# Performance work log

Measured on AMD Instinct MI355X. Metric: run time of the kernel, lower is better.

Reference implementation:

```python
import jax, jax.numpy as jnp
import numpy as np

H = 16          # ATTENTION_HEAD
E = 300         # EXPANSION_LENGTH
D = 768         # TEXT_EMBEDDING_DIM
HD = D // H     # 48


def setup_inputs() -> dict:
    key = jax.random.key(0)
    ks = jax.random.split(key, 10)
    b, n, ql, kl = 1, 4, 64, 64
    q = jax.random.normal(ks[0], (b, n, ql, D), dtype=jnp.float32)
    k = jax.random.normal(ks[1], (b, 1, kl, D), dtype=jnp.float32)
    v = jax.random.normal(ks[2], (b, 1, kl, D), dtype=jnp.float32)
    s = 1.0 / np.sqrt(D)
    Wq = jax.random.normal(ks[3], (D, D), dtype=jnp.float32) * s
    bq = jnp.zeros((D,), dtype=jnp.float32)
    Wk = jax.random.normal(ks[4], (D, D), dtype=jnp.float32) * s
    bk = jnp.zeros((D,), dtype=jnp.float32)
    Wv = jax.random.normal(ks[5], (D, D), dtype=jnp.float32) * s
    bv = jnp.zeros((D,), dtype=jnp.float32)
    memory = jax.random.normal(ks[6], (1, E, H, HD), dtype=jnp.float32) * 0.05
    return {"q": q, "k": k, "v": v, "Wq": Wq, "bq": bq, "Wk": Wk,
            "bk": bk, "Wv": Wv, "bv": bv, "memory": memory}


def reference(q, k, v, Wq, bq, Wk, bk, Wv, bv, memory):
    b, n, ql, _ = q.shape
    kl = k.shape[2]
    # Dense projections
    Q = (q @ Wq + bq).reshape(b, n, ql, H, HD)          # bnqhd
    K = (k @ Wk + bk).reshape(b, kl, H, HD)             # bkhd
    V = (v @ Wv + bv).reshape(b, kl, H, HD)             # bkhd
    # memory (1,E,H,HD) -> (1,E,1,H,HD); K -> (b,1,kl,H,HD); broadcast sum
    broad_sum = memory[:, :, None, :, :] + K[:, None, :, :, :]   # bekhd
    M = jax.nn.relu(jnp.einsum('bekhd,bnqhd->bnekqh', broad_sum, Q))
    E_seq = jnp.einsum('bnekqh,bkhd->bnekhd', M, V)
    out = jnp.einsum('bnekhd,bnekqh->bnqhd', E_seq, M)
    return out.reshape(q.shape)
```

## Files before the change

### kernel.cpp

```cpp
#include <hip/hip_runtime.h>

#define H   16
#define E   300
#define D   768
#define HD  48
#define QL  64
#define KL  64
#define NH  64
#define ROWS 384
#define SPLITK 12
#define NCH 16

#define OFF_PP 0
#define OFF_PF (SPLITK*ROWS*D)
#define OFF_A  (OFF_PF + ROWS*D)
#define OFF_B  (OFF_A + NH*E*QL)
#define OFF_SP (OFF_B + NH*KL*QL)

__global__ __launch_bounds__(256, 1) void proj_kernel(
    const float* __restrict__ qin, const float* __restrict__ kin, const float* __restrict__ vin,
    const float* __restrict__ Wq, const float* __restrict__ Wk, const float* __restrict__ Wv,
    float* __restrict__ ws)
{
    const int rowblk = blockIdx.x;
    const int col0   = blockIdx.y * 128;
    const int ks     = blockIdx.z;
    const int kbase  = ks * 64;

    const int g0 = rowblk * 128;
    const float* Wlo = (g0      < 256) ? Wq : (g0      < 320) ? Wk : Wv;
    const float* Whi = (g0 + 64 < 256) ? Wq : (g0 + 64 < 320) ? Wk : Wv;

    __shared__ float XsT[32][132];
    __shared__ float Ws2[2][32][128];

    const int tid = threadIdx.x;
    const int r0  = (tid >> 4) * 8;
    const int c0  = (tid & 15) * 8;
    const int hw  = r0 >> 6;

    float acc[8][8];
    #pragma unroll
    for (int i = 0; i < 8; i++)
        #pragma unroll
        for (int j = 0; j < 8; j++) acc[i][j] = 0.f;

    for (int kk2 = 0; kk2 < 64; kk2 += 32) {
        #pragma unroll
        for (int it = 0; it < 4; it++) {
            const int idx = it * 256 + tid;
            const int row = idx >> 3;
            const int d4  = (idx & 7) * 4;
            const int grow = rowblk * 128 + row;
            const float* src = (grow < 256) ? (qin + grow * D)
                             : (grow < 320) ? (kin + (grow - 256) * D)
                                            : (vin + (grow - 320) * D);
            const float4 xv = *(const float4*)(src + kbase + kk2 + d4);
            XsT[d4 + 0][row] = xv.x; XsT[d4 + 1][row] = xv.y;
            XsT[d4 + 2][row] = xv.z; XsT[d4 + 3][row] = xv.w;
        }
        #pragma unroll
        for (int it = 0; it < 8; it++) {
            const int idx  = it * 256 + tid;
            const int half = idx >> 10;
            const int rem  = idx & 1023;
            const int dk   = rem >> 5;
            const int c4   = (rem & 31) * 4;
            const float* Wsel = half ? Whi : Wlo;
            *(float4*)&Ws2[half][dk][c4] =
                *(const float4*)(Wsel + (kbase + kk2 + dk) * D + col0 + c4);
        }
        __syncthreads();
        #pragma unroll
        for (int dk = 0; dk < 32; dk++) {
            const float4 x0 = *(const float4*)&XsT[dk][r0];
            const float4 x1 = *(const float4*)&XsT[dk][r0 + 4];
            const float4 w0 = *(const float4*)&Ws2[hw][dk][c0];
            const float4 w1 = *(const float4*)&Ws2[hw][dk][c0 + 4];
            const float xr[8] = {x0.x, x0.y, x0.z, x0.w, x1.x, x1.y, x1.z, x1.w};
            const float wc[8] = {w0.x, w0.y, w0.z, w0.w, w1.x, w1.y, w1.z, w1.w};
            #pragma unroll
            for (int i = 0; i < 8; i++)
                #pragma unroll
                for (int j = 0; j < 8; j++)
                    acc[i][j] = fmaf(xr[i], wc[j], acc[i][j]);
        }
        __syncthreads();
    }
    float* P = ws + OFF_PP + ks * (ROWS * D);
    #pragma unroll
    for (int i = 0; i < 8; i++) {
        float* base = P + (rowblk * 128 + r0 + i) * D + col0 + c0;
        *(float4*)(base)     = make_float4(acc[i][0], acc[i][1], acc[i][2], acc[i][3]);
        *(float4*)(base + 4) = make_float4(acc[i][4], acc[i][5], acc[i][6], acc[i][7]);
    }
}

__global__ __launch_bounds__(256) void reduce_kernel(
    const float* __restrict__ bq, const float* __restrict__ bk, const float* __restrict__ bv,
    float* __restrict__ ws)
{
    const int idx = (blockIdx.x * 256 + threadIdx.x) * 4;
    const float* PP = ws + OFF_PP;
    float4 v = *(const float4*)(PP + idx);
    #pragma unroll
    for (int c = 1; c < SPLITK; c++) {
        const float4 p = *(const float4*)(PP + c * (ROWS * D) + idx);
        v.x += p.x; v.y += p.y; v.z += p.z; v.w += p.w;
    }
    const int row = idx / D, col = idx % D;
    const float* bias = (row < 256) ? bq : (row < 320) ? bk : bv;
    const float4 b = *(const float4*)(bias + col);
    v.x += b.x; v.y += b.y; v.z += b.z; v.w += b.w;
    *(float4*)(ws + OFF_PF + idx) = v;
}

__global__ __launch_bounds__(256) void ab_kernel(
    const float* __restrict__ memo, float* __restrict__ ws)
{
    const int nh = blockIdx.x;
    const int rg = blockIdx.y;
    const int n = nh >> 4, h = nh & 15;
    const float* Pf = ws + OFF_PF;
    float* A = ws + OFF_A;
    float* B = ws + OFF_B;

    __shared__ float RsT[48][132];
    __shared__ float QsT[48][68];

    const int tid = threadIdx.x;
    #pragma unroll
    for (int it = 0; it < 6; it++) {
        const int idx = it * 256 + tid;
        const int row = idx / 12;
        const int d4  = (idx % 12) * 4;
        const int rr = rg * 128 + row;
        float4 rv = make_float4(0.f, 0.f, 0.f, 0.f);
        if (rr < E)            rv = *(const float4*)(memo + rr * D + h * HD + d4);
        else if (rr < E + KL)  rv = *(const float4*)(Pf + (256 + rr - E) * D + h * HD + d4);
        RsT[d4 + 0][row] = rv.x; RsT[d4 + 1][row] = rv.y;
        RsT[d4 + 2][row] = rv.z; RsT[d4 + 3][row] = rv.w;
    }
    #pragma unroll
    for (int it = 0; it < 3; it++) {
        const int idx = it * 256 + tid;
        const int q  = idx / 12;
        const int d4 = (idx % 12) * 4;
        const float4 qv = *(const float4*)(Pf + (n * QL + q) * D + h * HD + d4);
        QsT[d4 + 0][q] = qv.x; QsT[d4 + 1][q] = qv.y;
        QsT[d4 + 2][q] = qv.z; QsT[d4 + 3][q] = qv.w;
    }
    __syncthreads();

    const int r0 = (tid >> 4) * 8;
    const int q0 = (tid & 15) * 4;
    float acc[8][4];
    #pragma unroll
    for (int i = 0; i < 8; i++)
        #pragma unroll
        for (int j = 0; j < 4; j++) acc[i][j] = 0.f;

    #pragma unroll 4
    for (int d = 0; d < HD; d++) {
        const float4 rf0 = *(const float4*)&RsT[d][r0];
        const float4 rf1 = *(const float4*)&RsT[d][r0 + 4];
        const float4 qf  = *(const float4*)&QsT[d][q0];
        const float rr8[8] = {rf0.x, rf0.y, rf0.z, rf0.w, rf1.x, rf1.y, rf1.z, rf1.w};
        const float qq4[4] = {qf.x, qf.y, qf.z, qf.w};
        #pragma unroll
        for (int i = 0; i < 8; i++)
            #pragma unroll
            for (int j = 0; j < 4; j++)
                acc[i][j] = fmaf(rr8[i], qq4[j], acc[i][j]);
    }
    #pragma unroll
    for (int i = 0; i < 8; i++) {
        const int rr = rg * 128 + r0 + i;
        const float4 av = make_float4(acc[i][0], acc[i][1], acc[i][2], acc[i][3]);
        if (rr < E)            *(float4*)(A + (nh * E + rr) * QL + q0) = av;
        else if (rr < E + KL)  *(float4*)(B + (nh * KL + (rr - E)) * QL + q0) = av;
    }
}

__global__ __launch_bounds__(256, 1) void main_kernel(float* __restrict__ ws)
{
    const int nh = blockIdx.x;
    const int cg = blockIdx.y;
    const int tid = threadIdx.x;
    const int lane = tid & 63;
    const int w = tid >> 6;

    __shared__ float As[75 * 64];
    __shared__ float Bs[64][68];

    const float* Ag = ws + OFF_A + (nh * E + cg * 75) * QL;
    for (int idx = tid; idx < 1200; idx += 256)
        *(float4*)&As[idx * 4] = *(const float4*)(Ag + idx * 4);
    const float* Bg = ws + OFF_B + nh * (KL * QL);
    #pragma unroll
    for (int it = 0; it < 4; it++) {
        const int idx = it * 256 + tid;
        const int k  = idx >> 4;
        const int q4 = (idx & 15) * 4;
        *(float4*)&Bs[k][q4] = *(const float4*)(Bg + idx * 4);
    }
    __syncthreads();

    float b[64];
    #pragma unroll
    for (int j = 0; j < 16; j++)
        *(float4*)&b[j * 4] = *(const float4*)&Bs[lane][j * 4];

    float s[64];
    #pragma unroll
    for (int j = 0; j < 64; j++) s[j] = 0.f;

    const int eBeg = w * 19;
    const int eEnd = (eBeg + 19 < 75) ? eBeg + 19 : 75;
    for (int e = eBeg; e < eEnd; e++) {
        float m[64];
        #pragma unroll
        for (int j4 = 0; j4 < 16; j4++) {
            const float4 a = *(const float4*)&As[e * 64 + j4 * 4];
            m[j4 * 4 + 0] = fmaxf(a.x + b[j4 * 4 + 0], 0.f);
            m[j4 * 4 + 1] = fmaxf(a.y + b[j4 * 4 + 1], 0.f);
            m[j4 * 4 + 2] = fmaxf(a.z + b[j4 * 4 + 2], 0.f);
            m[j4 * 4 + 3] = fmaxf(a.w + b[j4 * 4 + 3], 0.f);
        }
        float p0 = 0.f, p1 = 0.f, p2 = 0.f, p3 = 0.f;
        #pragma unroll
        for (int j4 = 0; j4 < 16; j4++) {
            p0 += m[j4 * 4 + 0]; p1 += m[j4 * 4 + 1];
            p2 += m[j4 * 4 + 2]; p3 += m[j4 * 4 + 3];
        }
        const float p = (p0 + p1) + (p2 + p3);
        #pragma unroll
        for (int j = 0; j < 64; j++)
            s[j] = fmaf(m[j], p, s[j]);
    }

    float* Sp = ws + OFF_SP + (((cg * 4 + w) * NH + nh) * QL) * KL;
    #pragma unroll
    for (int q = 0; q < 64; q++)
        Sp[q * KL + lane] = s[q];
}

__global__ __launch_bounds__(256) void out_kernel(
    const float* __restrict__ ws_c, float* __restrict__ outp)
{
    const int nh = blockIdx.x;
    const int qq = blockIdx.y;
    const int n = nh >> 4, h = nh & 15;
    const int q0 = qq * 16;
    const float* Sp = ws_c + OFF_SP;
    const float* Pf = ws_c + OFF_PF;

    __shared__ float S_l[16][64];
    __shared__ float V_l[64][52];

    const int tid = threadIdx.x;
    #pragma unroll
    for (int it = 0; it < 4; it++) {
        const int idx = it * 256 + tid;
        const int qi = idx >> 6, k = idx & 63;
        float sum = 0.f;
        #pragma unroll
        for (int c = 0; c < NCH; c++)
            sum += Sp[((c * NH + nh) * QL + q0 + qi) * KL + k];
        S_l[qi][k] = sum;
    }
    #pragma unroll
    for (int it = 0; it < 3; it++) {
        const int idx = it * 256 + tid;
        const int k  = idx / 12;
        const int d4 = (idx % 12) * 4;
        *(float4*)&V_l[k][d4] = *(const float4*)(Pf + (320 + k) * D + h * HD + d4);
    }
    __syncthreads();

    const int qi = tid >> 4;
    const int dg = tid & 15;
    if (dg < 12) {
        float a0 = 0.f, a1 = 0.f, a2 = 0.f, a3 = 0.f;
        #pragma unroll 8
        for (int k = 0; k < KL; k++) {
            const float sv = S_l[qi][k];
            const float4 vf = *(const float4*)&V_l[k][dg * 4];
            a0 = fmaf(sv, vf.x, a0); a1 = fmaf(sv, vf.y, a1);
            a2 = fmaf(sv, vf.z, a2); a3 = fmaf(sv, vf.w, a3);
        }
        *(float4*)(outp + (n * QL + q0 + qi) * D + h * HD + dg * 4) =
            make_float4(a0, a1, a2, a3);
    }
}

extern "C" void kernel_launch(void* const* d_in, const int* in_sizes, int n_in,
                              void* d_out, int out_size, void* d_ws, size_t ws_size,
                              hipStream_t stream)
{
    const float* q    = (const float*)d_in[0];
    const float* k    = (const float*)d_in[1];
    const float* v    = (const float*)d_in[2];
    const float* Wq   = (const float*)d_in[3];
    const float* bq   = (const float*)d_in[4];
    const float* Wk   = (const float*)d_in[5];
    const float* bk   = (const float*)d_in[6];
    const float* Wv   = (const float*)d_in[7];
    const float* bv   = (const float*)d_in[8];
    const float* memo = (const float*)d_in[9];
    float* ws   = (float*)d_ws;
    float* outp = (float*)d_out;

    hipLaunchKernelGGL(proj_kernel, dim3(3, 6, 12), dim3(256), 0, stream,
                       q, k, v, Wq, Wk, Wv, ws);
    hipLaunchKernelGGL(reduce_kernel, dim3(288), dim3(256), 0, stream, bq, bk, bv, ws);
    hipLaunchKernelGGL(ab_kernel, dim3(64, 3), dim3(256), 0, stream, memo, ws);
    hipLaunchKernelGGL(main_kernel, dim3(64, 4), dim3(256), 0, stream, ws);
    hipLaunchKernelGGL(out_kernel, dim3(64, 4), dim3(256), 0, stream, ws, outp);
}
```

Measured before the change: 124.5 us.

## Fuse split-K reduction into consumers and stream operands from global memory

Drops the separate reduce kernel. The split-K partial sums plus bias are now summed directly where Q, K and V are consumed, in the ab and out kernels. The projection kernel reads X rows directly from global memory instead of transposing them into shared memory. The ab kernel streams memory rows from global memory, and main_kernel reads A rows from global memory with double-buffered registers instead of staging them in shared memory. This removes one launch and a full write/read of the reduced projections, at the cost of redundant 12-way partial reads repeated across blocks and higher register pressure.

```diff
diff --git a/kernel.cpp b/kernel.cpp
--- a/kernel.cpp
+++ b/kernel.cpp
@@ -9,11 +9,10 @@
 #define NH  64
 #define ROWS 384
 #define SPLITK 12
-#define NCH 16
+#define NCHUNK 16
 
 #define OFF_PP 0
-#define OFF_PF (SPLITK*ROWS*D)
-#define OFF_A  (OFF_PF + ROWS*D)
+#define OFF_A  (SPLITK*ROWS*D)
 #define OFF_B  (OFF_A + NH*E*QL)
 #define OFF_SP (OFF_B + NH*KL*QL)
 
@@ -26,18 +25,27 @@
     const int col0   = blockIdx.y * 128;
     const int ks     = blockIdx.z;
     const int kbase  = ks * 64;
-
-    const int g0 = rowblk * 128;
-    const float* Wlo = (g0      < 256) ? Wq : (g0      < 320) ? Wk : Wv;
-    const float* Whi = (g0 + 64 < 256) ? Wq : (g0 + 64 < 320) ? Wk : Wv;
-
-    __shared__ float XsT[32][132];
+    const int g0     = rowblk * 128;
+
+    const float* Wlo = (g0      < 256) ? Wq : Wk;
+    const float* Whi = (g0 + 64 < 256) ? Wq : Wv;
+
     __shared__ float Ws2[2][32][128];
 
-    const int tid = threadIdx.x;
-    const int r0  = (tid >> 4) * 8;
-    const int c0  = (tid & 15) * 8;
-    const int hw  = r0 >> 6;
+    const int tid  = threadIdx.x;
+    const int half = tid >> 7;
+    const int loc  = tid & 127;
+    const int r0a  = (loc >> 4) * 4;
+    const int c0a  = (loc & 15) * 4;
+
+    const float* xp[8];
+    #pragma unroll
+    for (int i = 0; i < 8; i++) {
+        const int r = g0 + half * 64 + r0a + (i < 4 ? i : 28 + i);
+        xp[i] = ((r < 256) ? (qin + r * D)
+               : (r < 320) ? (kin + (r - 256) * D)
+                           : (vin + (r - 320) * D)) + kbase;
+    }
 
     float acc[8][8];
     #pragma unroll
@@ -47,140 +55,187 @@
 
     for (int kk2 = 0; kk2 < 64; kk2 += 32) {
         #pragma unroll
-        for (int it = 0; it < 4; it++) {
+        for (int it = 0; it < 8; it++) {
             const int idx = it * 256 + tid;
-            const int row = idx >> 3;
-            const int d4  = (idx & 7) * 4;
-            const int grow = rowblk * 128 + row;
-            const float* src = (grow < 256) ? (qin + grow * D)
-                             : (grow < 320) ? (kin + (grow - 256) * D)
-                                            : (vin + (grow - 320) * D);
-            const float4 xv = *(const float4*)(src + kbase + kk2 + d4);
-            XsT[d4 + 0][row] = xv.x; XsT[d4 + 1][row] = xv.y;
-            XsT[d4 + 2][row] = xv.z; XsT[d4 + 3][row] = xv.w;
-        }
-        #pragma unroll
-        for (int it = 0; it < 8; it++) {
-            const int idx  = it * 256 + tid;
-            const int half = idx >> 10;
-            const int rem  = idx & 1023;
-            const int dk   = rem >> 5;
-            const int c4   = (rem & 31) * 4;
-            const float* Wsel = half ? Whi : Wlo;
-            *(float4*)&Ws2[half][dk][c4] =
-                *(const float4*)(Wsel + (kbase + kk2 + dk) * D + col0 + c4);
+            const int s   = idx >> 10;
+            const int rem = idx & 1023;
+            const int dk  = rem >> 5;
+            const int c4  = (rem & 31) * 4;
+            *(float4*)&Ws2[s][dk][c4] =
+                *(const float4*)((s ? Whi : Wlo) + (kbase + kk2 + dk) * D + col0 + c4);
         }
         __syncthreads();
         #pragma unroll
-        for (int dk = 0; dk < 32; dk++) {
-            const float4 x0 = *(const float4*)&XsT[dk][r0];
-            const float4 x1 = *(const float4*)&XsT[dk][r0 + 4];
-            const float4 w0 = *(const float4*)&Ws2[hw][dk][c0];
-            const float4 w1 = *(const float4*)&Ws2[hw][dk][c0 + 4];
-            const float xr[8] = {x0.x, x0.y, x0.z, x0.w, x1.x, x1.y, x1.z, x1.w};
-            const float wc[8] = {w0.x, w0.y, w0.z, w0.w, w1.x, w1.y, w1.z, w1.w};
+        for (int dk4 = 0; dk4 < 8; dk4++) {
+            float4 xv[8];
             #pragma unroll
             for (int i = 0; i < 8; i++)
+                xv[i] = *(const float4*)(xp[i] + kk2 + dk4 * 4);
+            #pragma unroll
+            for (int t = 0; t < 4; t++) {
+                const float4 wa = *(const float4*)&Ws2[half][dk4 * 4 + t][c0a];
+                const float4 wb = *(const float4*)&Ws2[half][dk4 * 4 + t][c0a + 64];
+                const float wc[8] = {wa.x, wa.y, wa.z, wa.w, wb.x, wb.y, wb.z, wb.w};
                 #pragma unroll
-                for (int j = 0; j < 8; j++)
-                    acc[i][j] = fmaf(xr[i], wc[j], acc[i][j]);
+                for (int i = 0; i < 8; i++) {
+                    const float xs = ((const float*)&xv[i])[t];
+                    #pragma unroll
+                    for (int j = 0; j < 8; j++)
+                        acc[i][j] = fmaf(xs, wc[j], acc[i][j]);
+                }
+            }
         }
         __syncthreads();
     }
     float* P = ws + OFF_PP + ks * (ROWS * D);
     #pragma unroll
     for (int i = 0; i < 8; i++) {
-        float* base = P + (rowblk * 128 + r0 + i) * D + col0 + c0;
-        *(float4*)(base)     = make_float4(acc[i][0], acc[i][1], acc[i][2], acc[i][3]);
-        *(float4*)(base + 4) = make_float4(acc[i][4], acc[i][5], acc[i][6], acc[i][7]);
-    }
-}
-
-__global__ __launch_bounds__(256) void reduce_kernel(
-    const float* __restrict__ bq, const float* __restrict__ bk, const float* __restrict__ bv,
+        const int row = g0 + half * 64 + r0a + (i < 4 ? i : 28 + i);
+        *(float4*)(P + row * D + col0 + c0a) =
+            make_float4(acc[i][0], acc[i][1], acc[i][2], acc[i][3]);
+        *(float4*)(P + row * D + col0 + c0a + 64) =
+            make_float4(acc[i][4], acc[i][5], acc[i][6], acc[i][7]);
+    }
+}
+
+__global__ __launch_bounds__(256, 1) void ab_kernel(
+    const float* __restrict__ memo,
+    const float* __restrict__ bq_, const float* __restrict__ bk_,
     float* __restrict__ ws)
-{
-    const int idx = (blockIdx.x * 256 + threadIdx.x) * 4;
-    const float* PP = ws + OFF_PP;
-    float4 v = *(const float4*)(PP + idx);
-    #pragma unroll
-    for (int c = 1; c < SPLITK; c++) {
-        const float4 p = *(const float4*)(PP + c * (ROWS * D) + idx);
-        v.x += p.x; v.y += p.y; v.z += p.z; v.w += p.w;
-    }
-    const int row = idx / D, col = idx % D;
-    const float* bias = (row < 256) ? bq : (row < 320) ? bk : bv;
-    const float4 b = *(const float4*)(bias + col);
-    v.x += b.x; v.y += b.y; v.z += b.z; v.w += b.w;
-    *(float4*)(ws + OFF_PF + idx) = v;
-}
-
-__global__ __launch_bounds__(256) void ab_kernel(
-    const float* __restrict__ memo, float* __restrict__ ws)
 {
     const int nh = blockIdx.x;
     const int rg = blockIdx.y;
     const int n = nh >> 4, h = nh & 15;
-    const float* Pf = ws + OFF_PF;
+    const float* PP = ws + OFF_PP;
     float* A = ws + OFF_A;
     float* B = ws + OFF_B;
 
+    __shared__ float QsT[48][68];
     __shared__ float RsT[48][132];
-    __shared__ float QsT[48][68];
 
     const int tid = threadIdx.x;
-    #pragma unroll
-    for (int it = 0; it < 6; it++) {
-        const int idx = it * 256 + tid;
-        const int row = idx / 12;
-        const int d4  = (idx % 12) * 4;
-        const int rr = rg * 128 + row;
-        float4 rv = make_float4(0.f, 0.f, 0.f, 0.f);
-        if (rr < E)            rv = *(const float4*)(memo + rr * D + h * HD + d4);
-        else if (rr < E + KL)  rv = *(const float4*)(Pf + (256 + rr - E) * D + h * HD + d4);
-        RsT[d4 + 0][row] = rv.x; RsT[d4 + 1][row] = rv.y;
-        RsT[d4 + 2][row] = rv.z; RsT[d4 + 3][row] = rv.w;
-    }
-    #pragma unroll
-    for (int it = 0; it < 3; it++) {
-        const int idx = it * 256 + tid;
-        const int q  = idx / 12;
-        const int d4 = (idx % 12) * 4;
-        const float4 qv = *(const float4*)(Pf + (n * QL + q) * D + h * HD + d4);
-        QsT[d4 + 0][q] = qv.x; QsT[d4 + 1][q] = qv.y;
-        QsT[d4 + 2][q] = qv.z; QsT[d4 + 3][q] = qv.w;
+    for (int l = tid; l < 64 * 12; l += 256) {
+        const int q  = l / 12;
+        const int d4 = (l % 12) * 4;
+        float4 s = make_float4(0.f, 0.f, 0.f, 0.f);
+        #pragma unroll
+        for (int c = 0; c < SPLITK; c++) {
+            const float4 p = *(const float4*)(PP + c * (ROWS * D) + (n * QL + q) * D + h * HD + d4);
+            s.x += p.x; s.y += p.y; s.z += p.z; s.w += p.w;
+        }
+        const float4 bb = *(const float4*)(bq_ + h * HD + d4);
+        QsT[d4 + 0][q] = s.x + bb.x; QsT[d4 + 1][q] = s.y + bb.y;
+        QsT[d4 + 2][q] = s.z + bb.z; QsT[d4 + 3][q] = s.w + bb.w;
+    }
+    if (rg == 2) {
+        for (int l = tid; l < 128 * 12; l += 256) {
+            const int rr = l / 12;
+            const int d4 = (l % 12) * 4;
+            float4 s = make_float4(0.f, 0.f, 0.f, 0.f);
+            if (rr < 44) {
+                s = *(const float4*)(memo + ((256 + rr) * H + h) * HD + d4);
+            } else if (rr < 108) {
+                #pragma unroll
+                for (int c = 0; c < SPLITK; c++) {
+                    const float4 p = *(const float4*)(PP + c * (ROWS * D) + (256 + rr - 44) * D + h * HD + d4);
+                    s.x += p.x; s.y += p.y; s.z += p.z; s.w += p.w;
+                }
+                const float4 bb = *(const float4*)(bk_ + h * HD + d4);
+                s.x += bb.x; s.y += bb.y; s.z += bb.z; s.w += bb.w;
+            }
+            RsT[d4 + 0][rr] = s.x; RsT[d4 + 1][rr] = s.y;
+            RsT[d4 + 2][rr] = s.z; RsT[d4 + 3][rr] = s.w;
+        }
     }
     __syncthreads();
 
-    const int r0 = (tid >> 4) * 8;
-    const int q0 = (tid & 15) * 4;
+    const int r0a = (tid >> 4) * 4;
+    const int q0  = (tid & 15) * 4;
     float acc[8][4];
     #pragma unroll
     for (int i = 0; i < 8; i++)
         #pragma unroll
         for (int j = 0; j < 4; j++) acc[i][j] = 0.f;
 
-    #pragma unroll 4
-    for (int d = 0; d < HD; d++) {
-        const float4 rf0 = *(const float4*)&RsT[d][r0];
-        const float4 rf1 = *(const float4*)&RsT[d][r0 + 4];
-        const float4 qf  = *(const float4*)&QsT[d][q0];
-        const float rr8[8] = {rf0.x, rf0.y, rf0.z, rf0.w, rf1.x, rf1.y, rf1.z, rf1.w};
-        const float qq4[4] = {qf.x, qf.y, qf.z, qf.w};
-        #pragma unroll
-        for (int i = 0; i < 8; i++)
-            #pragma unroll
-            for (int j = 0; j < 4; j++)
-                acc[i][j] = fmaf(rr8[i], qq4[j], acc[i][j]);
-    }
+    if (rg < 2) {
+        const float* mp[8];
+        #pragma unroll
+        for (int i = 0; i < 8; i++) {
+            const int row = rg * 128 + r0a + (i < 4 ? i : 28 + i);
+            mp[i] = memo + (row * H + h) * HD;
+        }
+        #pragma unroll
+        for (int d4 = 0; d4 < 12; d4++) {
+            float4 xv[8];
+            #pragma unroll
+            for (int i = 0; i < 8; i++) xv[i] = *(const float4*)(mp[i] + d4 * 4);
+            #pragma unroll
+            for (int t = 0; t < 4; t++) {
+                const float4 qv = *(const float4*)&QsT[d4 * 4 + t][q0];
+                #pragma unroll
+                for (int i = 0; i < 8; i++) {
+                    const float xs = ((const float*)&xv[i])[t];
+                    acc[i][0] = fmaf(xs, qv.x, acc[i][0]);
+                    acc[i][1] = fmaf(xs, qv.y, acc[i][1]);
+                    acc[i][2] = fmaf(xs, qv.z, acc[i][2]);
+                    acc[i][3] = fmaf(xs, qv.w, acc[i][3]);
+                }
+            }
+        }
+    } else {
+        #pragma unroll 4
+        for (int d = 0; d < 48; d++) {
+            const float4 r0v = *(const float4*)&RsT[d][r0a];
+            const float4 r1v = *(const float4*)&RsT[d][r0a + 64];
+            const float4 qv  = *(const float4*)&QsT[d][q0];
+            const float rr8[8] = {r0v.x, r0v.y, r0v.z, r0v.w, r1v.x, r1v.y, r1v.z, r1v.w};
+            #pragma unroll
+            for (int i = 0; i < 8; i++) {
+                acc[i][0] = fmaf(rr8[i], qv.x, acc[i][0]);
+                acc[i][1] = fmaf(rr8[i], qv.y, acc[i][1]);
+                acc[i][2] = fmaf(rr8[i], qv.z, acc[i][2]);
+                acc[i][3] = fmaf(rr8[i], qv.w, acc[i][3]);
+            }
+        }
+    }
+
     #pragma unroll
     for (int i = 0; i < 8; i++) {
-        const int rr = rg * 128 + r0 + i;
+        const int rloc = r0a + (i < 4 ? i : 60 + i);
         const float4 av = make_float4(acc[i][0], acc[i][1], acc[i][2], acc[i][3]);
-        if (rr < E)            *(float4*)(A + (nh * E + rr) * QL + q0) = av;
-        else if (rr < E + KL)  *(float4*)(B + (nh * KL + (rr - E)) * QL + q0) = av;
-    }
-}
+        if (rg < 2) {
+            *(float4*)(A + (nh * E + rg * 128 + rloc) * QL + q0) = av;
+        } else {
+            if (rloc < 44)        *(float4*)(A + (nh * E + 256 + rloc) * QL + q0) = av;
+            else if (rloc < 108)  *(float4*)(B + (nh * KL + (rloc - 44)) * QL + q0) = av;
+        }
+    }
+}
+
+__device__ __forceinline__ void loadA16(float4* dst, const float* src) {
+    #pragma unroll
+    for (int j = 0; j < 16; j++) dst[j] = *(const float4*)(src + j * 4);
+}
+
+#define MAIN_STEP(AB) do {                                                  \
+    float m[64];                                                            \
+    _Pragma("unroll")                                                       \
+    for (int j4 = 0; j4 < 16; j4++) {                                       \
+        const float4 a = (AB)[j4];                                          \
+        m[j4*4+0] = fmaxf(a.x + b[j4*4+0], 0.f);                            \
+        m[j4*4+1] = fmaxf(a.y + b[j4*4+1], 0.f);                            \
+        m[j4*4+2] = fmaxf(a.z + b[j4*4+2], 0.f);                            \
+        m[j4*4+3] = fmaxf(a.w + b[j4*4+3], 0.f);                            \
+    }                                                                       \
+    float p0 = 0.f, p1 = 0.f, p2 = 0.f, p3 = 0.f;                           \
+    _Pragma("unroll")                                                       \
+    for (int j4 = 0; j4 < 16; j4++) {                                       \
+        p0 += m[j4*4+0]; p1 += m[j4*4+1]; p2 += m[j4*4+2]; p3 += m[j4*4+3]; \
+    }                                                                       \
+    const float p = (p0 + p1) + (p2 + p3);                                  \
+    _Pragma("unroll")                                                       \
+    for (int j = 0; j < 64; j++) s[j] = fmaf(m[j], p, s[j]);                \
+} while (0)
 
 __global__ __launch_bounds__(256, 1) void main_kernel(float* __restrict__ ws)
 {
@@ -189,92 +244,76 @@
     const int tid = threadIdx.x;
     const int lane = tid & 63;
     const int w = tid >> 6;
-
-    __shared__ float As[75 * 64];
-    __shared__ float Bs[64][68];
-
-    const float* Ag = ws + OFF_A + (nh * E + cg * 75) * QL;
-    for (int idx = tid; idx < 1200; idx += 256)
-        *(float4*)&As[idx * 4] = *(const float4*)(Ag + idx * 4);
-    const float* Bg = ws + OFF_B + nh * (KL * QL);
-    #pragma unroll
-    for (int it = 0; it < 4; it++) {
-        const int idx = it * 256 + tid;
-        const int k  = idx >> 4;
-        const int q4 = (idx & 15) * 4;
-        *(float4*)&Bs[k][q4] = *(const float4*)(Bg + idx * 4);
-    }
-    __syncthreads();
-
+    const int chunk = cg * 4 + w;
+    const int e0 = chunk * 19;
+    const int e1 = (e0 + 19 < E) ? e0 + 19 : E;
+
+    const float* Bg = ws + OFF_B + (nh * KL + lane) * QL;
     float b[64];
     #pragma unroll
     for (int j = 0; j < 16; j++)
-        *(float4*)&b[j * 4] = *(const float4*)&Bs[lane][j * 4];
+        *(float4*)&b[j * 4] = *(const float4*)(Bg + j * 4);
 
     float s[64];
     #pragma unroll
     for (int j = 0; j < 64; j++) s[j] = 0.f;
 
-    const int eBeg = w * 19;
-    const int eEnd = (eBeg + 19 < 75) ? eBeg + 19 : 75;
-    for (int e = eBeg; e < eEnd; e++) {
-        float m[64];
-        #pragma unroll
-        for (int j4 = 0; j4 < 16; j4++) {
-            const float4 a = *(const float4*)&As[e * 64 + j4 * 4];
-            m[j4 * 4 + 0] = fmaxf(a.x + b[j4 * 4 + 0], 0.f);
-            m[j4 * 4 + 1] = fmaxf(a.y + b[j4 * 4 + 1], 0.f);
-            m[j4 * 4 + 2] = fmaxf(a.z + b[j4 * 4 + 2], 0.f);
-            m[j4 * 4 + 3] = fmaxf(a.w + b[j4 * 4 + 3], 0.f);
-        }
-        float p0 = 0.f, p1 = 0.f, p2 = 0.f, p3 = 0.f;
-        #pragma unroll
-        for (int j4 = 0; j4 < 16; j4++) {
-            p0 += m[j4 * 4 + 0]; p1 += m[j4 * 4 + 1];
-            p2 += m[j4 * 4 + 2]; p3 += m[j4 * 4 + 3];
-        }
-        const float p = (p0 + p1) + (p2 + p3);
-        #pragma unroll
-        for (int j = 0; j < 64; j++)
-            s[j] = fmaf(m[j], p, s[j]);
-    }
-
-    float* Sp = ws + OFF_SP + (((cg * 4 + w) * NH + nh) * QL) * KL;
+    const float* Ag = ws + OFF_A + nh * (E * QL);
+    float4 A0[16], A1[16];
+    loadA16(A0, Ag + e0 * QL);
+    int e = e0;
+    while (true) {
+        if (e + 1 < e1) loadA16(A1, Ag + (e + 1) * QL);
+        MAIN_STEP(A0);
+        e++;
+        if (e >= e1) break;
+        if (e + 1 < e1) loadA16(A0, Ag + (e + 1) * QL);
+        MAIN_STEP(A1);
+        e++;
+        if (e >= e1) break;
+    }
+
+    float* Sp = ws + OFF_SP + (chunk * NH + nh) * (QL * KL);
     #pragma unroll
     for (int q = 0; q < 64; q++)
         Sp[q * KL + lane] = s[q];
 }
 
-__global__ __launch_bounds__(256) void out_kernel(
-    const float* __restrict__ ws_c, float* __restrict__ outp)
+__global__ __launch_bounds__(256, 1) void out_kernel(
+    const float* __restrict__ ws_c, const float* __restrict__ bv_, float* __restrict__ outp)
 {
     const int nh = blockIdx.x;
     const int qq = blockIdx.y;
     const int n = nh >> 4, h = nh & 15;
     const int q0 = qq * 16;
     const float* Sp = ws_c + OFF_SP;
-    const float* Pf = ws_c + OFF_PF;
-
-    __shared__ float S_l[16][64];
+    const float* PP = ws_c + OFF_PP;
+
+    __shared__ float S_l[16][65];
     __shared__ float V_l[64][52];
 
     const int tid = threadIdx.x;
+    for (int l = tid; l < 64 * 12; l += 256) {
+        const int k  = l / 12;
+        const int d4 = (l % 12) * 4;
+        float4 s = make_float4(0.f, 0.f, 0.f, 0.f);
+        #pragma unroll
+        for (int c = 0; c < SPLITK; c++) {
+            const float4 p = *(const float4*)(PP + c * (ROWS * D) + (320 + k) * D + h * HD + d4);
+            s.x += p.x; s.y += p.y; s.z += p.z; s.w += p.w;
+        }
+        const float4 bb = *(const float4*)(bv_ + h * HD + d4);
+        *(float4*)&V_l[k][d4] = make_float4(s.x + bb.x, s.y + bb.y, s.z + bb.z, s.w + bb.w);
+    }
     #pragma unroll
     for (int it = 0; it < 4; it++) {
         const int idx = it * 256 + tid;
         const int qi = idx >> 6, k = idx & 63;
         float sum = 0.f;
         #pragma unroll
-        for (int c = 0; c < NCH; c++)
+        for (int c = 0; c < NCHUNK; c++)
             sum += Sp[((c * NH + nh) * QL + q0 + qi) * KL + k];
         S_l[qi][k] = sum;
-    }
-    #pragma unroll
-    for (int it = 0; it < 3; it++) {
-        const int idx = it * 256 + tid;
-        const int k  = idx / 12;
-        const int d4 = (idx % 12) * 4;
-        *(float4*)&V_l[k][d4] = *(const float4*)(Pf + (320 + k) * D + h * HD + d4);
     }
     __syncthreads();
 
@@ -313,8 +352,7 @@
 
     hipLaunchKernelGGL(proj_kernel, dim3(3, 6, 12), dim3(256), 0, stream,
                        q, k, v, Wq, Wk, Wv, ws);
-    hipLaunchKernelGGL(reduce_kernel, dim3(288), dim3(256), 0, stream, bq, bk, bv, ws);
-    hipLaunchKernelGGL(ab_kernel, dim3(64, 3), dim3(256), 0, stream, memo, ws);
+    hipLaunchKernelGGL(ab_kernel, dim3(64, 3), dim3(256), 0, stream, memo, bq, bk, ws);
     hipLaunchKernelGGL(main_kernel, dim3(64, 4), dim3(256), 0, stream, ws);
-    hipLaunchKernelGGL(out_kernel, dim3(64, 4), dim3(256), 0, stream, ws, outp);
-}
+    hipLaunchKernelGGL(out_kernel, dim3(64, 4), dim3(256), 0, stream, ws, bv, outp);
+}
```

After: 157.9 us. +26.8%, slower.

## Fuse all stages into one cooperative persistent kernel with grid syncs

Applied to the files above, without the earlier changes.

Replaces the five back-to-back launches with a single cooperative kernel of 256 blocks that runs projection, split-K reduction, A/B products, the main accumulation and the output stage, separated by grid.sync(). The aim is to remove per-launch overhead and the idle gaps between kernels, using a shared-memory union so each phase reuses the same LDS. The projection thread mapping is also reworked so each half of the block handles one weight half, with strided rows and columns. A fallback path folds the reduction into ab_kernel and out_kernel in case the cooperative launch fails. Grid-wide barriers carry their own cost and force all 256 blocks to be co-resident.

```diff
diff --git a/kernel.cpp b/kernel.cpp
--- a/kernel.cpp
+++ b/kernel.cpp
@@ -1,4 +1,7 @@
 #include <hip/hip_runtime.h>
+#include <hip/hip_cooperative_groups.h>
+
+namespace cg = cooperative_groups;
 
 #define H   16
 #define E   300
@@ -9,13 +12,14 @@
 #define NH  64
 #define ROWS 384
 #define SPLITK 12
-#define NCH 16
+#define NCHUNK 16
 
 #define OFF_PP 0
 #define OFF_PF (SPLITK*ROWS*D)
 #define OFF_A  (OFF_PF + ROWS*D)
 #define OFF_B  (OFF_A + NH*E*QL)
 #define OFF_SP (OFF_B + NH*KL*QL)
+
 
 __global__ __launch_bounds__(256, 1) void proj_kernel(
     const float* __restrict__ qin, const float* __restrict__ kin, const float* __restrict__ vin,
@@ -26,18 +30,19 @@
     const int col0   = blockIdx.y * 128;
     const int ks     = blockIdx.z;
     const int kbase  = ks * 64;
-
-    const int g0 = rowblk * 128;
-    const float* Wlo = (g0      < 256) ? Wq : (g0      < 320) ? Wk : Wv;
-    const float* Whi = (g0 + 64 < 256) ? Wq : (g0 + 64 < 320) ? Wk : Wv;
+    const int g0     = rowblk * 128;
+
+    const float* Wlo = (g0      < 256) ? Wq : Wk;
+    const float* Whi = (g0 + 64 < 256) ? Wq : Wv;
 
     __shared__ float XsT[32][132];
     __shared__ float Ws2[2][32][128];
 
-    const int tid = threadIdx.x;
-    const int r0  = (tid >> 4) * 8;
-    const int c0  = (tid & 15) * 8;
-    const int hw  = r0 >> 6;
+    const int tid  = threadIdx.x;
+    const int half = tid >> 7;
+    const int loc  = tid & 127;
+    const int r0a  = (loc >> 4) * 4;
+    const int c0a  = (loc & 15) * 4;
 
     float acc[8][8];
     #pragma unroll
@@ -51,7 +56,7 @@
             const int idx = it * 256 + tid;
             const int row = idx >> 3;
             const int d4  = (idx & 7) * 4;
-            const int grow = rowblk * 128 + row;
+            const int grow = g0 + row;
             const float* src = (grow < 256) ? (qin + grow * D)
                              : (grow < 320) ? (kin + (grow - 256) * D)
                                             : (vin + (grow - 320) * D);
@@ -61,24 +66,23 @@
         }
         #pragma unroll
         for (int it = 0; it < 8; it++) {
-            const int idx  = it * 256 + tid;
-            const int half = idx >> 10;
-            const int rem  = idx & 1023;
-            const int dk   = rem >> 5;
-            const int c4   = (rem & 31) * 4;
-            const float* Wsel = half ? Whi : Wlo;
-            *(float4*)&Ws2[half][dk][c4] =
-                *(const float4*)(Wsel + (kbase + kk2 + dk) * D + col0 + c4);
+            const int idx = it * 256 + tid;
+            const int s   = idx >> 10;
+            const int rem = idx & 1023;
+            const int dk  = rem >> 5;
+            const int c4  = (rem & 31) * 4;
+            *(float4*)&Ws2[s][dk][c4] =
+                *(const float4*)((s ? Whi : Wlo) + (kbase + kk2 + dk) * D + col0 + c4);
         }
         __syncthreads();
         #pragma unroll
         for (int dk = 0; dk < 32; dk++) {
-            const float4 x0 = *(const float4*)&XsT[dk][r0];
-            const float4 x1 = *(const float4*)&XsT[dk][r0 + 4];
-            const float4 w0 = *(const float4*)&Ws2[hw][dk][c0];
-            const float4 w1 = *(const float4*)&Ws2[hw][dk][c0 + 4];
-            const float xr[8] = {x0.x, x0.y, x0.z, x0.w, x1.x, x1.y, x1.z, x1.w};
-            const float wc[8] = {w0.x, w0.y, w0.z, w0.w, w1.x, w1.y, w1.z, w1.w};
+            const float4 xa = *(const float4*)&XsT[dk][half * 64 + r0a];
+            const float4 xb = *(const float4*)&XsT[dk][half * 64 + r0a + 32];
+            const float4 wa = *(const float4*)&Ws2[half][dk][c0a];
+            const float4 wb = *(const float4*)&Ws2[half][dk][c0a + 64];
+            const float xr[8] = {xa.x, xa.y, xa.z, xa.w, xb.x, xb.y, xb.z, xb.w};
+            const float wc[8] = {wa.x, wa.y, wa.z, wa.w, wb.x, wb.y, wb.z, wb.w};
             #pragma unroll
             for (int i = 0; i < 8; i++)
                 #pragma unroll
@@ -90,65 +94,61 @@
     float* P = ws + OFF_PP + ks * (ROWS * D);
     #pragma unroll
     for (int i = 0; i < 8; i++) {
-        float* base = P + (rowblk * 128 + r0 + i) * D + col0 + c0;
-        *(float4*)(base)     = make_float4(acc[i][0], acc[i][1], acc[i][2], acc[i][3]);
-        *(float4*)(base + 4) = make_float4(acc[i][4], acc[i][5], acc[i][6], acc[i][7]);
+        const int row = g0 + half * 64 + r0a + (i < 4 ? i : 28 + i);
+        *(float4*)(P + row * D + col0 + c0a) =
+            make_float4(acc[i][0], acc[i][1], acc[i][2], acc[i][3]);
+        *(float4*)(P + row * D + col0 + c0a + 64) =
+            make_float4(acc[i][4], acc[i][5], acc[i][6], acc[i][7]);
     }
 }
 
-__global__ __launch_bounds__(256) void reduce_kernel(
-    const float* __restrict__ bq, const float* __restrict__ bk, const float* __restrict__ bv,
+__global__ __launch_bounds__(256, 1) void ab_kernel(
+    const float* __restrict__ memo,
+    const float* __restrict__ bq_, const float* __restrict__ bk_,
     float* __restrict__ ws)
-{
-    const int idx = (blockIdx.x * 256 + threadIdx.x) * 4;
-    const float* PP = ws + OFF_PP;
-    float4 v = *(const float4*)(PP + idx);
-    #pragma unroll
-    for (int c = 1; c < SPLITK; c++) {
-        const float4 p = *(const float4*)(PP + c * (ROWS * D) + idx);
-        v.x += p.x; v.y += p.y; v.z += p.z; v.w += p.w;
-    }
-    const int row = idx / D, col = idx % D;
-    const float* bias = (row < 256) ? bq : (row < 320) ? bk : bv;
-    const float4 b = *(const float4*)(bias + col);
-    v.x += b.x; v.y += b.y; v.z += b.z; v.w += b.w;
-    *(float4*)(ws + OFF_PF + idx) = v;
-}
-
-__global__ __launch_bounds__(256) void ab_kernel(
-    const float* __restrict__ memo, float* __restrict__ ws)
 {
     const int nh = blockIdx.x;
     const int rg = blockIdx.y;
     const int n = nh >> 4, h = nh & 15;
-    const float* Pf = ws + OFF_PF;
+    const float* PP = ws + OFF_PP;
     float* A = ws + OFF_A;
     float* B = ws + OFF_B;
 
+    __shared__ float QsT[48][68];
     __shared__ float RsT[48][132];
-    __shared__ float QsT[48][68];
 
     const int tid = threadIdx.x;
-    #pragma unroll
-    for (int it = 0; it < 6; it++) {
-        const int idx = it * 256 + tid;
-        const int row = idx / 12;
-        const int d4  = (idx % 12) * 4;
-        const int rr = rg * 128 + row;
-        float4 rv = make_float4(0.f, 0.f, 0.f, 0.f);
-        if (rr < E)            rv = *(const float4*)(memo + rr * D + h * HD + d4);
-        else if (rr < E + KL)  rv = *(const float4*)(Pf + (256 + rr - E) * D + h * HD + d4);
-        RsT[d4 + 0][row] = rv.x; RsT[d4 + 1][row] = rv.y;
-        RsT[d4 + 2][row] = rv.z; RsT[d4 + 3][row] = rv.w;
-    }
-    #pragma unroll
-    for (int it = 0; it < 3; it++) {
-        const int idx = it * 256 + tid;
-        const int q  = idx / 12;
-        const int d4 = (idx % 12) * 4;
-        const float4 qv = *(const float4*)(Pf + (n * QL + q) * D + h * HD + d4);
-        QsT[d4 + 0][q] = qv.x; QsT[d4 + 1][q] = qv.y;
-        QsT[d4 + 2][q] = qv.z; QsT[d4 + 3][q] = qv.w;
+    for (int l = tid; l < 64 * 12; l += 256) {
+        const int q  = l / 12;
+        const int d4 = (l % 12) * 4;
+        float4 s = make_float4(0.f, 0.f, 0.f, 0.f);
+        #pragma unroll
+        for (int c = 0; c < SPLITK; c++) {
+            const float4 p = *(const float4*)(PP + c * (ROWS * D) + (n * QL + q) * D + h * HD + d4);
+            s.x += p.x; s.y += p.y; s.z += p.z; s.w += p.w;
+        }
+        const float4 bb = *(const float4*)(bq_ + h * HD + d4);
+        QsT[d4 + 0][q] = s.x + bb.x; QsT[d4 + 1][q] = s.y + bb.y;
+        QsT[d4 + 2][q] = s.z + bb.z; QsT[d4 + 3][q] = s.w + bb.w;
+    }
+    for (int l = tid; l < 128 * 12; l += 256) {
+        const int row = l / 12;
+        const int d4  = (l % 12) * 4;
+        const int rr  = rg * 128 + row;
+        float4 s = make_float4(0.f, 0.f, 0.f, 0.f);
+        if (rr < E) {
+            s = *(const float4*)(memo + rr * D + h * HD + d4);
+        } else if (rr < E + KL) {
+            #pragma unroll
+            for (int c = 0; c < SPLITK; c++) {
+                const float4 p = *(const float4*)(PP + c * (ROWS * D) + (256 + rr - E) * D + h * HD + d4);
+                s.x += p.x; s.y += p.y; s.z += p.z; s.w += p.w;
+            }
+            const float4 bb = *(const float4*)(bk_ + h * HD + d4);
+            s.x += bb.x; s.y += bb.y; s.z += bb.z; s.w += bb.w;
+        }
+        RsT[d4 + 0][row] = s.x; RsT[d4 + 1][row] = s.y;
+        RsT[d4 + 2][row] = s.z; RsT[d4 + 3][row] = s.w;
     }
     __syncthreads();
 
@@ -166,12 +166,13 @@
         const float4 rf1 = *(const float4*)&RsT[d][r0 + 4];
         const float4 qf  = *(const float4*)&QsT[d][q0];
         const float rr8[8] = {rf0.x, rf0.y, rf0.z, rf0.w, rf1.x, rf1.y, rf1.z, rf1.w};
-        const float qq4[4] = {qf.x, qf.y, qf.z, qf.w};
-        #pragma unroll
-        for (int i = 0; i < 8; i++)
-            #pragma unroll
-            for (int j = 0; j < 4; j++)
-                acc[i][j] = fmaf(rr8[i], qq4[j], acc[i][j]);
+        #pragma unroll
+        for (int i = 0; i < 8; i++) {
+            acc[i][0] = fmaf(rr8[i], qf.x, acc[i][0]);
+            acc[i][1] = fmaf(rr8[i], qf.y, acc[i][1]);
+            acc[i][2] = fmaf(rr8[i], qf.z, acc[i][2]);
+            acc[i][3] = fmaf(rr8[i], qf.w, acc[i][3]);
+        }
     }
     #pragma unroll
     for (int i = 0; i < 8; i++) {
@@ -185,7 +186,7 @@
 __global__ __launch_bounds__(256, 1) void main_kernel(float* __restrict__ ws)
 {
     const int nh = blockIdx.x;
-    const int cg = blockIdx.y;
+    const int cgI = blockIdx.y;
     const int tid = threadIdx.x;
     const int lane = tid & 63;
     const int w = tid >> 6;
@@ -193,7 +194,7 @@
     __shared__ float As[75 * 64];
     __shared__ float Bs[64][68];
 
-    const float* Ag = ws + OFF_A + (nh * E + cg * 75) * QL;
+    const float* Ag = ws + OFF_A + (nh * E + cgI * 75) * QL;
     for (int idx = tid; idx < 1200; idx += 256)
         *(float4*)&As[idx * 4] = *(const float4*)(Ag + idx * 4);
     const float* Bg = ws + OFF_B + nh * (KL * QL);
@@ -239,42 +240,47 @@
             s[j] = fmaf(m[j], p, s[j]);
     }
 
-    float* Sp = ws + OFF_SP + (((cg * 4 + w) * NH + nh) * QL) * KL;
+    float* Sp = ws + OFF_SP + ((cgI * 4 + w) * NH + nh) * (QL * KL);
     #pragma unroll
     for (int q = 0; q < 64; q++)
         Sp[q * KL + lane] = s[q];
 }
 
-__global__ __launch_bounds__(256) void out_kernel(
-    const float* __restrict__ ws_c, float* __restrict__ outp)
+__global__ __launch_bounds__(256, 1) void out_kernel(
+    const float* __restrict__ ws_c, const float* __restrict__ bv_, float* __restrict__ outp)
 {
     const int nh = blockIdx.x;
     const int qq = blockIdx.y;
     const int n = nh >> 4, h = nh & 15;
     const int q0 = qq * 16;
     const float* Sp = ws_c + OFF_SP;
-    const float* Pf = ws_c + OFF_PF;
-
-    __shared__ float S_l[16][64];
+    const float* PP = ws_c + OFF_PP;
+
+    __shared__ float S_l[16][65];
     __shared__ float V_l[64][52];
 
     const int tid = threadIdx.x;
+    for (int l = tid; l < 64 * 12; l += 256) {
+        const int k  = l / 12;
+        const int d4 = (l % 12) * 4;
+        float4 s = make_float4(0.f, 0.f, 0.f, 0.f);
+        #pragma unroll
+        for (int c = 0; c < SPLITK; c++) {
+            const float4 p = *(const float4*)(PP + c * (ROWS * D) + (320 + k) * D + h * HD + d4);
+            s.x += p.x; s.y += p.y; s.z += p.z; s.w += p.w;
+        }
+        const float4 bb = *(const float4*)(bv_ + h * HD + d4);
+        *(float4*)&V_l[k][d4] = make_float4(s.x + bb.x, s.y + bb.y, s.z + bb.z, s.w + bb.w);
+    }
     #pragma unroll
     for (int it = 0; it < 4; it++) {
         const int idx = it * 256 + tid;
         const int qi = idx >> 6, k = idx & 63;
         float sum = 0.f;
         #pragma unroll
-        for (int c = 0; c < NCH; c++)
+        for (int c = 0; c < NCHUNK; c++)
             sum += Sp[((c * NH + nh) * QL + q0 + qi) * KL + k];
         S_l[qi][k] = sum;
-    }
-    #pragma unroll
-    for (int it = 0; it < 3; it++) {
-        const int idx = it * 256 + tid;
-        const int k  = idx / 12;
-        const int d4 = (idx % 12) * 4;
-        *(float4*)&V_l[k][d4] = *(const float4*)(Pf + (320 + k) * D + h * HD + d4);
     }
     __syncthreads();
 
@@ -291,6 +297,284 @@
         }
         *(float4*)(outp + (n * QL + q0 + qi) * D + h * HD + dg * 4) =
             make_float4(a0, a1, a2, a3);
+    }
+}
+
+__global__ __launch_bounds__(256, 1) void fused_kernel(
+    const float* __restrict__ qin, const float* __restrict__ kin, const float* __restrict__ vin,
+    const float* __restrict__ Wq, const float* __restrict__ bq_,
+    const float* __restrict__ Wk, const float* __restrict__ bk_,
+    const float* __restrict__ Wv, const float* __restrict__ bv_,
+    const float* __restrict__ memo, float* __restrict__ ws, float* __restrict__ outp)
+{
+    cg::grid_group grid = cg::this_grid();
+
+    __shared__ union SU {
+        struct { float XsT[32][132]; float Ws2[2][32][128]; } p1;
+        struct { float QsT[48][68];  float RsT[48][132];    } p3;
+        struct { float As[75 * 64];  float Bs[64][68];      } p4;
+        struct { float S_l[16][65];  float V_l[64][52];     } p5;
+    } sm;
+
+    const int bid = blockIdx.x;
+    const int tid = threadIdx.x;
+
+    if (bid < 216) {
+        const int ks     = bid / 18;
+        const int rc     = bid % 18;
+        const int rowblk = rc / 6;
+        const int col0   = (rc % 6) * 128;
+        const int kbase  = ks * 64;
+        const int g0     = rowblk * 128;
+        const float* Wlo = (g0      < 256) ? Wq : Wk;
+        const float* Whi = (g0 + 64 < 256) ? Wq : Wv;
+
+        const int half = tid >> 7;
+        const int loc  = tid & 127;
+        const int r0a  = (loc >> 4) * 4;
+        const int c0a  = (loc & 15) * 4;
+
+        float acc[8][8];
+        #pragma unroll
+        for (int i = 0; i < 8; i++)
+            #pragma unroll
+            for (int j = 0; j < 8; j++) acc[i][j] = 0.f;
+
+        for (int kk2 = 0; kk2 < 64; kk2 += 32) {
+            #pragma unroll
+            for (int it = 0; it < 4; it++) {
+                const int idx = it * 256 + tid;
+                const int row = idx >> 3;
+                const int d4  = (idx & 7) * 4;
+                const int grow = g0 + row;
+                const float* src = (grow < 256) ? (qin + grow * D)
+                                 : (grow < 320) ? (kin + (grow - 256) * D)
+                                                : (vin + (grow - 320) * D);
+                const float4 xv = *(const float4*)(src + kbase + kk2 + d4);
+                sm.p1.XsT[d4 + 0][row] = xv.x; sm.p1.XsT[d4 + 1][row] = xv.y;
+                sm.p1.XsT[d4 + 2][row] = xv.z; sm.p1.XsT[d4 + 3][row] = xv.w;
+            }
+            #pragma unroll
+            for (int it = 0; it < 8; it++) {
+                const int idx = it * 256 + tid;
+                const int s   = idx >> 10;
+                const int rem = idx & 1023;
+                const int dk  = rem >> 5;
+                const int c4  = (rem & 31) * 4;
+                *(float4*)&sm.p1.Ws2[s][dk][c4] =
+                    *(const float4*)((s ? Whi : Wlo) + (kbase + kk2 + dk) * D + col0 + c4);
+            }
+            __syncthreads();
+            #pragma unroll
+            for (int dk = 0; dk < 32; dk++) {
+                const float4 xa = *(const float4*)&sm.p1.XsT[dk][half * 64 + r0a];
+                const float4 xb = *(const float4*)&sm.p1.XsT[dk][half * 64 + r0a + 32];
+                const float4 wa = *(const float4*)&sm.p1.Ws2[half][dk][c0a];
+                const float4 wb = *(const float4*)&sm.p1.Ws2[half][dk][c0a + 64];
+                const float xr[8] = {xa.x, xa.y, xa.z, xa.w, xb.x, xb.y, xb.z, xb.w};
+                const float wc[8] = {wa.x, wa.y, wa.z, wa.w, wb.x, wb.y, wb.z, wb.w};
+                #pragma unroll
+                for (int i = 0; i < 8; i++)
+                    #pragma unroll
+                    for (int j = 0; j < 8; j++)
+                        acc[i][j] = fmaf(xr[i], wc[j], acc[i][j]);
+            }
+            __syncthreads();
+        }
+        float* P = ws + OFF_PP + ks * (ROWS * D);
+        #pragma unroll
+        for (int i = 0; i < 8; i++) {
+            const int row = g0 + half * 64 + r0a + (i < 4 ? i : 28 + i);
+            *(float4*)(P + row * D + col0 + c0a) =
+                make_float4(acc[i][0], acc[i][1], acc[i][2], acc[i][3]);
+            *(float4*)(P + row * D + col0 + c0a + 64) =
+                make_float4(acc[i][4], acc[i][5], acc[i][6], acc[i][7]);
+        }
+    }
+    grid.sync();
+
+    for (int i4 = bid * 256 + tid; i4 < (ROWS * D) / 4; i4 += 65536) {
+        const int idx = i4 * 4;
+        const float* PP = ws + OFF_PP;
+        float4 v = *(const float4*)(PP + idx);
+        #pragma unroll
+        for (int c = 1; c < SPLITK; c++) {
+            const float4 p = *(const float4*)(PP + c * (ROWS * D) + idx);
+            v.x += p.x; v.y += p.y; v.z += p.z; v.w += p.w;
+        }
+        const int row = idx / D, col = idx % D;
+        const float* bias = (row < 256) ? bq_ : (row < 320) ? bk_ : bv_;
+        const float4 b = *(const float4*)(bias + col);
+        v.x += b.x; v.y += b.y; v.z += b.z; v.w += b.w;
+        *(float4*)(ws + OFF_PF + idx) = v;
+    }
+    grid.sync();
+
+    if (bid < 192) {
+        const int nh = bid & 63;
+        const int rg = bid >> 6;
+        const int n = nh >> 4, h = nh & 15;
+        const float* Pf = ws + OFF_PF;
+        float* A = ws + OFF_A;
+        float* B = ws + OFF_B;
+
+        #pragma unroll
+        for (int it = 0; it < 6; it++) {
+            const int idx = it * 256 + tid;
+            const int row = idx / 12;
+            const int d4  = (idx % 12) * 4;
+            const int rr = rg * 128 + row;
+            float4 rv = make_float4(0.f, 0.f, 0.f, 0.f);
+            if (rr < E)            rv = *(const float4*)(memo + rr * D + h * HD + d4);
+            else if (rr < E + KL)  rv = *(const float4*)(Pf + (256 + rr - E) * D + h * HD + d4);
+            sm.p3.RsT[d4 + 0][row] = rv.x; sm.p3.RsT[d4 + 1][row] = rv.y;
+            sm.p3.RsT[d4 + 2][row] = rv.z; sm.p3.RsT[d4 + 3][row] = rv.w;
+        }
+        #pragma unroll
+        for (int it = 0; it < 3; it++) {
+            const int idx = it * 256 + tid;
+            const int q  = idx / 12;
+            const int d4 = (idx % 12) * 4;
+            const float4 qv = *(const float4*)(Pf + (n * QL + q) * D + h * HD + d4);
+            sm.p3.QsT[d4 + 0][q] = qv.x; sm.p3.QsT[d4 + 1][q] = qv.y;
+            sm.p3.QsT[d4 + 2][q] = qv.z; sm.p3.QsT[d4 + 3][q] = qv.w;
+        }
+        __syncthreads();
+
+        const int r0 = (tid >> 4) * 8;
+        const int q0 = (tid & 15) * 4;
+        float acc[8][4];
+        #pragma unroll
+        for (int i = 0; i < 8; i++)
+            #pragma unroll
+            for (int j = 0; j < 4; j++) acc[i][j] = 0.f;
+
+        #pragma unroll 4
+        for (int d = 0; d < HD; d++) {
+            const float4 rf0 = *(const float4*)&sm.p3.RsT[d][r0];
+            const float4 rf1 = *(const float4*)&sm.p3.RsT[d][r0 + 4];
+            const float4 qf  = *(const float4*)&sm.p3.QsT[d][q0];
+            const float rr8[8] = {rf0.x, rf0.y, rf0.z, rf0.w, rf1.x, rf1.y, rf1.z, rf1.w};
+            #pragma unroll
+            for (int i = 0; i < 8; i++) {
+                acc[i][0] = fmaf(rr8[i], qf.x, acc[i][0]);
+                acc[i][1] = fmaf(rr8[i], qf.y, acc[i][1]);
+                acc[i][2] = fmaf(rr8[i], qf.z, acc[i][2]);
+                acc[i][3] = fmaf(rr8[i], qf.w, acc[i][3]);
+            }
+        }
+        #pragma unroll
+        for (int i = 0; i < 8; i++) {
+            const int rr = rg * 128 + r0 + i;
+            const float4 av = make_float4(acc[i][0], acc[i][1], acc[i][2], acc[i][3]);
+            if (rr < E)            *(float4*)(A + (nh * E + rr) * QL + q0) = av;
+            else if (rr < E + KL)  *(float4*)(B + (nh * KL + (rr - E)) * QL + q0) = av;
+        }
+        __syncthreads();
+    }
+    grid.sync();
+
+    {
+        const int nh = bid & 63;
+        const int cgI = bid >> 6;
+        const int lane = tid & 63;
+        const int w = tid >> 6;
+
+        const float* Ag = ws + OFF_A + (nh * E + cgI * 75) * QL;
+        for (int idx = tid; idx < 1200; idx += 256)
+            *(float4*)&sm.p4.As[idx * 4] = *(const float4*)(Ag + idx * 4);
+        const float* Bg = ws + OFF_B + nh * (KL * QL);
+        #pragma unroll
+        for (int it = 0; it < 4; it++) {
+            const int idx = it * 256 + tid;
+            const int k  = idx >> 4;
+            const int q4 = (idx & 15) * 4;
+            *(float4*)&sm.p4.Bs[k][q4] = *(const float4*)(Bg + idx * 4);
+        }
+        __syncthreads();
+
+        float b[64];
+        #pragma unroll
+        for (int j = 0; j < 16; j++)
+            *(float4*)&b[j * 4] = *(const float4*)&sm.p4.Bs[lane][j * 4];
+
+        float s[64];
+        #pragma unroll
+        for (int j = 0; j < 64; j++) s[j] = 0.f;
+
+        const int eBeg = w * 19;
+        const int eEnd = (eBeg + 19 < 75) ? eBeg + 19 : 75;
+        for (int e = eBeg; e < eEnd; e++) {
+            float m[64];
+            #pragma unroll
+            for (int j4 = 0; j4 < 16; j4++) {
+                const float4 a = *(const float4*)&sm.p4.As[e * 64 + j4 * 4];
+                m[j4 * 4 + 0] = fmaxf(a.x + b[j4 * 4 + 0], 0.f);
+                m[j4 * 4 + 1] = fmaxf(a.y + b[j4 * 4 + 1], 0.f);
+                m[j4 * 4 + 2] = fmaxf(a.z + b[j4 * 4 + 2], 0.f);
+                m[j4 * 4 + 3] = fmaxf(a.w + b[j4 * 4 + 3], 0.f);
+            }
+            float p0 = 0.f, p1 = 0.f, p2 = 0.f, p3 = 0.f;
+            #pragma unroll
+            for (int j4 = 0; j4 < 16; j4++) {
+                p0 += m[j4 * 4 + 0]; p1 += m[j4 * 4 + 1];
+                p2 += m[j4 * 4 + 2]; p3 += m[j4 * 4 + 3];
+            }
+            const float p = (p0 + p1) + (p2 + p3);
+            #pragma unroll
+            for (int j = 0; j < 64; j++)
+                s[j] = fmaf(m[j], p, s[j]);
+        }
+
+        float* Sp = ws + OFF_SP + ((cgI * 4 + w) * NH + nh) * (QL * KL);
+        #pragma unroll
+        for (int q = 0; q < 64; q++)
+            Sp[q * KL + lane] = s[q];
+        __syncthreads();
+    }
+    grid.sync();
+
+    {
+        const int nh = bid & 63;
+        const int qq = bid >> 6;
+        const int n = nh >> 4, h = nh & 15;
+        const int q0 = qq * 16;
+        const float* Sp = ws + OFF_SP;
+        const float* Pf = ws + OFF_PF;
+
+        #pragma unroll
+        for (int it = 0; it < 3; it++) {
+            const int idx = it * 256 + tid;
+            const int k  = idx / 12;
+            const int d4 = (idx % 12) * 4;
+            *(float4*)&sm.p5.V_l[k][d4] = *(const float4*)(Pf + (320 + k) * D + h * HD + d4);
+        }
+        #pragma unroll
+        for (int it = 0; it < 4; it++) {
+            const int idx = it * 256 + tid;
+            const int qi = idx >> 6, k = idx & 63;
+            float sum = 0.f;
+            #pragma unroll
+            for (int c = 0; c < NCHUNK; c++)
+                sum += Sp[((c * NH + nh) * QL + q0 + qi) * KL + k];
+            sm.p5.S_l[qi][k] = sum;
+        }
+        __syncthreads();
+
+        const int qi = tid >> 4;
+        const int dg = tid & 15;
+        if (dg < 12) {
+            float a0 = 0.f, a1 = 0.f, a2 = 0.f, a3 = 0.f;
+            #pragma unroll 8
+            for (int k = 0; k < KL; k++) {
+                const float sv = sm.p5.S_l[qi][k];
+                const float4 vf = *(const float4*)&sm.p5.V_l[k][dg * 4];
+                a0 = fmaf(sv, vf.x, a0); a1 = fmaf(sv, vf.y, a1);
+                a2 = fmaf(sv, vf.z, a2); a3 = fmaf(sv, vf.w, a3);
+            }
+            *(float4*)(outp + (n * QL + q0 + qi) * D + h * HD + dg * 4) =
+                make_float4(a0, a1, a2, a3);
+        }
     }
 }
 
@@ -311,10 +595,19 @@
     float* ws   = (float*)d_ws;
     float* outp = (float*)d_out;
 
-    hipLaunchKernelGGL(proj_kernel, dim3(3, 6, 12), dim3(256), 0, stream,
-                       q, k, v, Wq, Wk, Wv, ws);
-    hipLaunchKernelGGL(reduce_kernel, dim3(288), dim3(256), 0, stream, bq, bk, bv, ws);
-    hipLaunchKernelGGL(ab_kernel, dim3(64, 3), dim3(256), 0, stream, memo, ws);
-    hipLaunchKernelGGL(main_kernel, dim3(64, 4), dim3(256), 0, stream, ws);
-    hipLaunchKernelGGL(out_kernel, dim3(64, 4), dim3(256), 0, stream, ws, outp);
+    void* args[] = {
+        (void*)&q, (void*)&k, (void*)&v,
+        (void*)&Wq, (void*)&bq, (void*)&Wk, (void*)&bk, (void*)&Wv, (void*)&bv,
+        (void*)&memo, (void*)&ws, (void*)&outp
+    };
+    hipError_t err = hipLaunchCooperativeKernel((const void*)fused_kernel,
+                                                dim3(256), dim3(256), args, 0, stream);
+    if (err != hipSuccess) {
+        (void)hipGetLastError();
+        hipLaunchKernelGGL(proj_kernel, dim3(3, 6, 12), dim3(256), 0, stream,
+                           q, k, v, Wq, Wk, Wv, ws);
+        hipLaunchKernelGGL(ab_kernel, dim3(64, 3), dim3(256), 0, stream, memo, bq, bk, ws);
+        hipLaunchKernelGGL(main_kernel, dim3(64, 4), dim3(256), 0, stream, ws);
+        hipLaunchKernelGGL(out_kernel, dim3(64, 4), dim3(256), 0, stream, ws, bv, outp);
+    }
 }
```

New measurement: 288.0 us. 131% more time.
